# Performance work log

Measured on AMD Instinct MI355X. Metric: run time of the kernel, lower is better.

## Reference

```python
import jax, jax.numpy as jnp
import numpy as np

B, S = 256, 512
V, E, H, O = 256, 128, 256, 128


def setup_inputs() -> dict:
    key = jax.random.key(0)
    ks = jax.random.split(key, 8)
    s_e = 1.0 / np.sqrt(H)
    return {
        "x": jax.random.randint(ks[0], (B, S), 0, V),
        "emb": jax.random.normal(ks[1], (V, E), dtype=jnp.float32),
        "W_ih": jax.random.uniform(ks[2], (4 * H, E), jnp.float32, -s_e, s_e),
        "W_hh": jax.random.uniform(ks[3], (4 * H, H), jnp.float32, -s_e, s_e),
        "b_ih": jax.random.uniform(ks[4], (4 * H,), jnp.float32, -s_e, s_e),
        "b_hh": jax.random.uniform(ks[5], (4 * H,), jnp.float32, -s_e, s_e),
        "W_out": jax.random.uniform(ks[6], (O, H), jnp.float32, -s_e, s_e),
        "b_out": jax.random.uniform(ks[7], (O,), jnp.float32, -s_e, s_e),
    }


def _lstm_last_h(xe, W_ih, W_hh, b_ih, b_hh):
    # xe: [B, S, E]. Precompute input contribution to all gates: [S, B, 4H]
    pre = jnp.einsum("bse,ge->sbg", xe, W_ih) + (b_ih + b_hh)
    Bn = xe.shape[0]
    h0 = jnp.zeros((Bn, H), xe.dtype)
    c0 = jnp.zeros((Bn, H), xe.dtype)

    def step(carry, p):
        h, c = carry
        gates = p + h @ W_hh.T  # [B, 4H]
        i, f, g, o = jnp.split(gates, 4, axis=-1)  # PyTorch gate order i,f,g,o
        i = jax.nn.sigmoid(i)
        f = jax.nn.sigmoid(f)
        g = jnp.tanh(g)
        o = jax.nn.sigmoid(o)
        c = f * c + i * g
        h = o * jnp.tanh(c)
        return (h, c), None

    (h, _), _ = jax.lax.scan(step, (h0, c0), pre)
    return h  # [B, H] == lstm output at last timestep


def reference(x, emb, W_ih, W_hh, b_ih, b_hh, W_out, b_out):
    xe = emb[x]  # [B, S, E] embedding lookup
    h_last = _lstm_last_h(xe, W_ih, W_hh, b_ih, b_hh)
    return h_last @ W_out.T + b_out  # [B, O]
```

## Files before the change

kernel.cpp:

```cpp
#include <hip/hip_runtime.h>


typedef _Float16 f16x8 __attribute__((ext_vector_type(8)));
typedef _Float16 f16x4 __attribute__((ext_vector_type(4)));
typedef float    f32x4 __attribute__((ext_vector_type(4)));

#define B_  256
#define S_  512
#define V_  256
#define E_  128
#define H_  256
#define O_  128

#define T_OFF     0u
#define HLAST_OFF (512u << 10)
#define WPK_OFF   (768u << 10)

__global__ void build_table(const float* __restrict__ emb,
                            const float* __restrict__ W_ih,
                            const float* __restrict__ b_ih,
                            const float* __restrict__ b_hh,
                            _Float16* __restrict__ T2h) {
    const int v   = blockIdx.x;
    const int tid = threadIdx.x;

    __shared__ float e[E_];
    if (tid < E_) e[tid] = emb[v * E_ + tid];
    __syncthreads();

    f16x4 tv;
#pragma unroll
    for (int t = 0; t < 4; ++t) {
        const int g = t * 256 + tid;
        const float4* wp = (const float4*)(W_ih + g * E_);
        float acc = 0.f;
#pragma unroll
        for (int i = 0; i < E_ / 4; ++i) {
            float4 w = wp[i];
            acc += w.x * e[4*i] + w.y * e[4*i+1] + w.z * e[4*i+2] + w.w * e[4*i+3];
        }
        tv[t] = (_Float16)(acc + b_ih[g] + b_hh[g]);
    }
    *(f16x4*)(T2h + ((size_t)v * 256 + tid) * 4) = tv;
}

__global__ void prepack(const float* __restrict__ W_hh,
                        _Float16* __restrict__ Wpk) {
    const int blk = blockIdx.x;
    const int ktS = blk >> 3;
    const int j   = blk & 7;
    const int kt  = 6 + ktS;
    const int tid = threadIdx.x;
    const int wv = tid >> 6, l = tid & 63, l15 = l & 15, quad = l >> 4;
    const int n  = j * 128 + wv * 16 + l15;
    const int k0 = kt * 32 + quad * 8;
    const float4* wp = (const float4*)(W_hh + (size_t)n * H_ + k0);
    float4 w0 = wp[0];
    float4 w1 = wp[1];
    f16x8 f = (f16x8){
        (_Float16)w0.x, (_Float16)w0.y, (_Float16)w0.z, (_Float16)w0.w,
        (_Float16)w1.x, (_Float16)w1.y, (_Float16)w1.z, (_Float16)w1.w};
    *(f16x8*)(Wpk + ((size_t)blk * 512 + tid) * 8) = f;
}

__device__ __forceinline__ float sig_fast(float x) {
    float t = __builtin_amdgcn_exp2f(-1.4426950408889634f * x);
    return __builtin_amdgcn_rcpf(1.f + t);
}
__device__ __forceinline__ float tanh_fast(float x) {
    x = fminf(fmaxf(x, -30.f), 30.f);
    float t = __builtin_amdgcn_exp2f(-2.8853900817779268f * x);
    return (1.f - t) * __builtin_amdgcn_rcpf(1.f + t);
}

#define HSTRIDE 272

__launch_bounds__(512, 2)
__global__ void lstm_persistent(const int* __restrict__ x,
                                const float* __restrict__ W_hh,
                                const _Float16* __restrict__ T2h,
                                const _Float16* __restrict__ Wpk,
                                float* __restrict__ hlast) {
    const int tid    = threadIdx.x;
    const int wv     = tid >> 6;
    const int l      = tid & 63;
    const int l15    = l & 15;
    const int quad   = l >> 4;
    const int stripe = blockIdx.x;
    const int uu     = wv * 16 + l15;

    __shared__ __align__(16) _Float16 wlds[8][8][2][512];
    __shared__ __align__(16) _Float16 hbuf[2][4][HSTRIDE];
    __shared__ __align__(16) _Float16 zbuf[256];

    if (tid < 128) ((int*)zbuf)[tid] = 0;

    f16x8 wreg[8][4];
#pragma unroll
    for (int j = 0; j < 8; ++j) {
        const float* wr = W_hh + (size_t)(j * 128 + uu) * H_ + quad * 8;
#pragma unroll
        for (int kt = 0; kt < 6; ++kt) {
            const float4* wp = (const float4*)(wr + kt * 32);
            float4 w0 = wp[0];
            float4 w1 = wp[1];
            f16x8 f = (f16x8){
                (_Float16)w0.x, (_Float16)w0.y, (_Float16)w0.z, (_Float16)w0.w,
                (_Float16)w1.x, (_Float16)w1.y, (_Float16)w1.z, (_Float16)w1.w};
            if (kt < 2)
                *(f16x8*)&wlds[wv][j][kt][(size_t)l * 8] = f;
            else
                wreg[j][kt - 2] = f;
        }
    }

    const int grow = stripe * 4 + quad;
    float c2[2] = {0.f, 0.f};

    int xv = x[(size_t)grow * S_];

    f16x8 wstr[4][2];

    __syncthreads();

    for (int s = 0; s < S_; ++s) {
        f16x4 tcv[2];
        tcv[0] = *(const f16x4*)(T2h + ((size_t)xv * 256 + uu) * 4);
        tcv[1] = *(const f16x4*)(T2h + ((size_t)xv * 256 + uu + 128) * 4);
        if (s + 1 < S_) xv = x[(size_t)grow * S_ + s + 1];

        f32x4 acc[8];
#pragma unroll
        for (int j = 0; j < 8; ++j) acc[j] = (f32x4){0.f, 0.f, 0.f, 0.f};

        if (s > 0) {
            const _Float16* ha = ((l15 & 3) == 0)
                ? (&hbuf[(s - 1) & 1][l15 >> 2][0] + quad * 8)
                : (zbuf + quad * 8);

#pragma unroll
            for (int pass = 0; pass < 2; ++pass) {
#pragma unroll
                for (int kt = 0; kt < 8; ++kt) {
                    f16x8 a = *(const f16x8*)(ha + kt * 32);
                    if (kt < 2) {
#pragma unroll
                        for (int jj = 0; jj < 4; ++jj) {
                            f16x8 b = *(const f16x8*)
                                &wlds[wv][pass * 4 + jj][kt][(size_t)l * 8];
                            acc[pass * 4 + jj] =
                                __builtin_amdgcn_mfma_f32_16x16x32_f16(
                                    a, b, acc[pass * 4 + jj], 0, 0, 0);
                        }
                    } else if (kt < 6) {
#pragma unroll
                        for (int jj = 0; jj < 4; ++jj)
                            acc[pass * 4 + jj] =
                                __builtin_amdgcn_mfma_f32_16x16x32_f16(
                                    a, wreg[pass * 4 + jj][kt - 2],
                                    acc[pass * 4 + jj], 0, 0, 0);
                    } else {
#pragma unroll
                        for (int jj = 0; jj < 4; ++jj)
                            acc[pass * 4 + jj] =
                                __builtin_amdgcn_mfma_f32_16x16x32_f16(
                                    a, wstr[jj][kt - 6],
                                    acc[pass * 4 + jj], 0, 0, 0);
                    }
                }
                if (pass == 0) {
#pragma unroll
                    for (int jj = 0; jj < 4; ++jj)
#pragma unroll
                        for (int ktS = 0; ktS < 2; ++ktS)
                            wstr[jj][ktS] = *(const f16x8*)(
                                Wpk + ((size_t)((ktS * 8 + 4 + jj) * 512 + tid)) * 8);
                }
            }
        }

        const bool last = (s == S_ - 1);
#pragma unroll
        for (int p = 0; p < 2; ++p) {
            float gi = sig_fast (acc[0 + p][0] + (float)tcv[p][0]);
            float gf = sig_fast (acc[2 + p][0] + (float)tcv[p][1]);
            float gg = tanh_fast(acc[4 + p][0] + (float)tcv[p][2]);
            float go = sig_fast (acc[6 + p][0] + (float)tcv[p][3]);
            float cc = gf * c2[p] + gi * gg;
            c2[p] = cc;
            float hv = go * tanh_fast(cc);
            if (!last) {
                hbuf[s & 1][quad][uu + p * 128] = (_Float16)hv;
            } else {
                hlast[(size_t)grow * H_ + uu + p * 128] = hv;
            }
        }

        if (!last) {
#pragma unroll
            for (int jj = 0; jj < 4; ++jj)
#pragma unroll
                for (int ktS = 0; ktS < 2; ++ktS)
                    wstr[jj][ktS] = *(const f16x8*)(
                        Wpk + ((size_t)((ktS * 8 + jj) * 512 + tid)) * 8);
        }

        __syncthreads();
    }
}

__global__ void out_kernel(const float* __restrict__ hlast,
                           const float* __restrict__ W_out,
                           const float* __restrict__ b_out,
                           float* __restrict__ out) {
    const int b = blockIdx.x;
    const int o = threadIdx.x;
    __shared__ float hl[H_];
    hl[o]       = hlast[b * H_ + o];
    hl[o + 128] = hlast[b * H_ + o + 128];
    __syncthreads();
    const float4* wp = (const float4*)(W_out + o * H_);
    float acc = 0.f;
#pragma unroll
    for (int i = 0; i < H_ / 4; ++i) {
        float4 w = wp[i];
        acc += w.x * hl[4*i] + w.y * hl[4*i+1] + w.z * hl[4*i+2] + w.w * hl[4*i+3];
    }
    out[b * O_ + o] = acc + b_out[o];
}

extern "C" void kernel_launch(void* const* d_in, const int* in_sizes, int n_in,
                              void* d_out, int out_size, void* d_ws, size_t ws_size,
                              hipStream_t stream) {
    const int*   x     = (const int*)  d_in[0];
    const float* emb   = (const float*)d_in[1];
    const float* W_ih  = (const float*)d_in[2];
    const float* W_hh  = (const float*)d_in[3];
    const float* b_ih  = (const float*)d_in[4];
    const float* b_hh  = (const float*)d_in[5];
    const float* W_out = (const float*)d_in[6];
    const float* b_out = (const float*)d_in[7];
    float* out = (float*)d_out;

    char* ws = (char*)d_ws;
    _Float16* T2h   = (_Float16*)(ws + T_OFF);
    float*    hlast = (float*)(ws + HLAST_OFF);
    _Float16* Wpk   = (_Float16*)(ws + WPK_OFF);

    build_table<<<dim3(V_), dim3(256), 0, stream>>>(emb, W_ih, b_ih, b_hh, T2h);
    prepack<<<dim3(16), dim3(512), 0, stream>>>(W_hh, Wpk);
    lstm_persistent<<<dim3(64), dim3(512), 0, stream>>>(x, W_hh, T2h, Wpk, hlast);
    out_kernel<<<dim3(B_), dim3(O_), 0, stream>>>(hlast, W_out, b_out, out);
}
```

Measured before the change: 896.1 us.

## Restructure W_hh k-tile streaming to hide global load latency mid-step

The split of W_hh k-tiles changes: streamed tiles are now kt=3 and kt=7 instead of kt=6,7, and the register-resident tiles become kt=2,4,5,6. The MFMA loop is reordered to iterate k-tiles outer over all 8 gate blocks, so the streamed tile for kt=3 (loaded at the end of the previous step) is consumed early. The kt=7 loads are issued right after it, behind a sched_barrier, so they overlap with the register-tile MFMAs. This aims to hide the L2 latency of the per-step streamed weights, at the cost of a fixed schedule and eight live streamed registers instead of four pairs.

```diff
diff --git a/kernel.cpp b/kernel.cpp
--- a/kernel.cpp
+++ b/kernel.cpp
@@ -49,7 +49,7 @@
     const int blk = blockIdx.x;
     const int ktS = blk >> 3;
     const int j   = blk & 7;
-    const int kt  = 6 + ktS;
+    const int kt  = 3 + ktS * 4;
     const int tid = threadIdx.x;
     const int wv = tid >> 6, l = tid & 63, l15 = l & 15, quad = l >> 4;
     const int n  = j * 128 + wv * 16 + l15;
@@ -100,7 +100,8 @@
     for (int j = 0; j < 8; ++j) {
         const float* wr = W_hh + (size_t)(j * 128 + uu) * H_ + quad * 8;
 #pragma unroll
-        for (int kt = 0; kt < 6; ++kt) {
+        for (int kt = 0; kt < 7; ++kt) {
+            if (kt == 3) continue;
             const float4* wp = (const float4*)(wr + kt * 32);
             float4 w0 = wp[0];
             float4 w1 = wp[1];
@@ -110,7 +111,7 @@
             if (kt < 2)
                 *(f16x8*)&wlds[wv][j][kt][(size_t)l * 8] = f;
             else
-                wreg[j][kt - 2] = f;
+                wreg[j][(kt == 2) ? 0 : kt - 3] = f;
         }
     }
 
@@ -119,7 +120,8 @@
 
     int xv = x[(size_t)grow * S_];
 
-    f16x8 wstr[4][2];
+    f16x8 wstr[8];
+    const _Float16* wpk_lane = Wpk + (size_t)tid * 8;
 
     __syncthreads();
 
@@ -139,43 +141,49 @@
                 : (zbuf + quad * 8);
 
 #pragma unroll
-            for (int pass = 0; pass < 2; ++pass) {
-#pragma unroll
-                for (int kt = 0; kt < 8; ++kt) {
-                    f16x8 a = *(const f16x8*)(ha + kt * 32);
-                    if (kt < 2) {
-#pragma unroll
-                        for (int jj = 0; jj < 4; ++jj) {
-                            f16x8 b = *(const f16x8*)
-                                &wlds[wv][pass * 4 + jj][kt][(size_t)l * 8];
-                            acc[pass * 4 + jj] =
-                                __builtin_amdgcn_mfma_f32_16x16x32_f16(
-                                    a, b, acc[pass * 4 + jj], 0, 0, 0);
-                        }
-                    } else if (kt < 6) {
-#pragma unroll
-                        for (int jj = 0; jj < 4; ++jj)
-                            acc[pass * 4 + jj] =
-                                __builtin_amdgcn_mfma_f32_16x16x32_f16(
-                                    a, wreg[pass * 4 + jj][kt - 2],
-                                    acc[pass * 4 + jj], 0, 0, 0);
-                    } else {
-#pragma unroll
-                        for (int jj = 0; jj < 4; ++jj)
-                            acc[pass * 4 + jj] =
-                                __builtin_amdgcn_mfma_f32_16x16x32_f16(
-                                    a, wstr[jj][kt - 6],
-                                    acc[pass * 4 + jj], 0, 0, 0);
-                    }
+            for (int kt = 0; kt < 2; ++kt) {
+                f16x8 a = *(const f16x8*)(ha + kt * 32);
+#pragma unroll
+                for (int j = 0; j < 8; ++j) {
+                    f16x8 b = *(const f16x8*)&wlds[wv][j][kt][(size_t)l * 8];
+                    acc[j] = __builtin_amdgcn_mfma_f32_16x16x32_f16(
+                        a, b, acc[j], 0, 0, 0);
                 }
-                if (pass == 0) {
-#pragma unroll
-                    for (int jj = 0; jj < 4; ++jj)
-#pragma unroll
-                        for (int ktS = 0; ktS < 2; ++ktS)
-                            wstr[jj][ktS] = *(const f16x8*)(
-                                Wpk + ((size_t)((ktS * 8 + 4 + jj) * 512 + tid)) * 8);
-                }
+            }
+            {
+                f16x8 a = *(const f16x8*)(ha + 2 * 32);
+#pragma unroll
+                for (int j = 0; j < 8; ++j)
+                    acc[j] = __builtin_amdgcn_mfma_f32_16x16x32_f16(
+                        a, wreg[j][0], acc[j], 0, 0, 0);
+            }
+            {
+                f16x8 a = *(const f16x8*)(ha + 3 * 32);
+#pragma unroll
+                for (int j = 0; j < 8; ++j)
+                    acc[j] = __builtin_amdgcn_mfma_f32_16x16x32_f16(
+                        a, wstr[j], acc[j], 0, 0, 0);
+            }
+
+            __builtin_amdgcn_sched_barrier(0);
+#pragma unroll
+            for (int j = 0; j < 8; ++j)
+                wstr[j] = *(const f16x8*)(wpk_lane + ((size_t)(8 + j) * 512) * 8);
+
+#pragma unroll
+            for (int m = 1; m < 4; ++m) {
+                f16x8 a = *(const f16x8*)(ha + (m + 3) * 32);
+#pragma unroll
+                for (int j = 0; j < 8; ++j)
+                    acc[j] = __builtin_amdgcn_mfma_f32_16x16x32_f16(
+                        a, wreg[j][m], acc[j], 0, 0, 0);
+            }
+            {
+                f16x8 a = *(const f16x8*)(ha + 7 * 32);
+#pragma unroll
+                for (int j = 0; j < 8; ++j)
+                    acc[j] = __builtin_amdgcn_mfma_f32_16x16x32_f16(
+                        a, wstr[j], acc[j], 0, 0, 0);
             }
         }
 
@@ -198,11 +206,8 @@
 
         if (!last) {
 #pragma unroll
-            for (int jj = 0; jj < 4; ++jj)
-#pragma unroll
-                for (int ktS = 0; ktS < 2; ++ktS)
-                    wstr[jj][ktS] = *(const f16x8*)(
-                        Wpk + ((size_t)((ktS * 8 + jj) * 512 + tid)) * 8);
+            for (int j = 0; j < 8; ++j)
+                wstr[j] = *(const f16x8*)(wpk_lane + ((size_t)j * 512) * 8);
         }
 
         __syncthreads();
```

Result: faster. 863.5 us (-3.6%).
